# Kernel optimization log

Hardware: AMD Instinct MI355X
Metric: run time of the kernel (lower is better)

The kernel has to match this reference:

```python
import jax, jax.numpy as jnp
import numpy as np

B, T, D, E = 8, 512, 128, 256

def setup_inputs() -> dict:
    key = jax.random.key(0)
    ks = jax.random.split(key, 6)
    s_d = 1.0 / np.sqrt(D)
    return {
        "x": jax.random.normal(ks[0], (B, T, D), jnp.float32),
        "Wg": jax.random.normal(ks[1], (D, E), jnp.float32) * s_d,
        "bg": jnp.zeros((E,), jnp.float32),
        "expert_w": jax.random.normal(ks[2], (E, D, D), jnp.float32) * s_d,
        "w1": jax.random.normal(ks[3], (D, D), jnp.float32) * s_d,
        "b1": jnp.zeros((D,), jnp.float32),
        "w2": jax.random.normal(ks[4], (D, D), jnp.float32) * s_d,
        "b2": jnp.zeros((D,), jnp.float32),
    }

def reference(x, Wg, bg, expert_w, w1, b1, w2, b2):
    n_experts = expert_w.shape[0]
    # router (context=None -> route on x itself)
    gate_scores = jax.nn.softmax(x @ Wg + bg, axis=-1)            # [B,T,E]
    top_vals, top_idx = jax.lax.top_k(gate_scores, 2)             # [B,T,2]
    top_w = top_vals / (jnp.sum(top_vals, axis=-1, keepdims=True) + 1e-6)
    # dense per-expert projection (faithful to original einsum over ALL experts)
    expert_outputs = jnp.einsum('btd,edo->bteo', x, expert_w)     # [B,T,E,D]
    # top-2 one-hot mask with normalized weights -> [B,T,E]
    mask = jnp.sum(jax.nn.one_hot(top_idx, n_experts, dtype=x.dtype) * top_w[..., None], axis=2)
    mixed = jnp.einsum('bteo,bte->bto', expert_outputs, mask)     # [B,T,D]
    # SwiGLU
    g = mixed @ w1 + b1
    weighted_avg = g * jax.nn.sigmoid(g) * (mixed @ w2 + b2)      # [B,T,D]
    # variance consensus against swiglu output
    diff_sq = jnp.square(expert_outputs - weighted_avg[:, :, None, :])
    weighted_var = jnp.einsum('bteo,bte->bto', diff_sq, mask)     # [B,T,D]
    consensus = jnp.exp(-jnp.mean(weighted_var, axis=-1))         # [B,T]
    return weighted_avg, consensus
```

## Files before the change

### kernel.cpp

```cpp
#include <hip/hip_runtime.h>
#include <math.h>

#define NT  4096
#define DD  128
#define EE  256

__global__ __launch_bounds__(256) void router_kernel(
    const float* __restrict__ x, const float* __restrict__ Wg,
    const float* __restrict__ bg, float2* __restrict__ ww,
    int2* __restrict__ sel)
{
    const int bid = blockIdx.x;
    const int tid = threadIdx.x;
    const int t0  = bid * 8;

    __shared__ float xt[DD][8];
    __shared__ float lg[8][EE];

    {
        const int q = tid >> 5, part = tid & 31;
        const float4 v = *(reinterpret_cast<const float4*>(
            x + (size_t)(t0 + q) * DD) + part);
        xt[part * 4 + 0][q] = v.x;
        xt[part * 4 + 1][q] = v.y;
        xt[part * 4 + 2][q] = v.z;
        xt[part * 4 + 3][q] = v.w;
    }
    __syncthreads();

    {
        const int e = tid;
        const float be = bg[e];
        float a0 = be, a1 = be, a2 = be, a3 = be;
        float a4 = be, a5 = be, a6 = be, a7 = be;
        #pragma unroll 8
        for (int d = 0; d < DD; ++d) {
            const float w = Wg[(size_t)d * EE + e];
            const float4 xa = *reinterpret_cast<const float4*>(&xt[d][0]);
            const float4 xb = *reinterpret_cast<const float4*>(&xt[d][4]);
            a0 = fmaf(xa.x, w, a0);  a1 = fmaf(xa.y, w, a1);
            a2 = fmaf(xa.z, w, a2);  a3 = fmaf(xa.w, w, a3);
            a4 = fmaf(xb.x, w, a4);  a5 = fmaf(xb.y, w, a5);
            a6 = fmaf(xb.z, w, a6);  a7 = fmaf(xb.w, w, a7);
        }
        lg[0][e] = a0;  lg[1][e] = a1;  lg[2][e] = a2;  lg[3][e] = a3;
        lg[4][e] = a4;  lg[5][e] = a5;  lg[6][e] = a6;  lg[7][e] = a7;
    }
    __syncthreads();

    const int lane = tid & 63;
    const int wv   = tid >> 6;
    #pragma unroll
    for (int rep = 0; rep < 2; ++rep) {
        const int tk = wv * 2 + rep;
        const int t  = t0 + tk;
        const float4 lv = *reinterpret_cast<const float4*>(&lg[tk][lane * 4]);
        float v[4] = {lv.x, lv.y, lv.z, lv.w};

        float m = v[0]; int mi = lane * 4;
        #pragma unroll
        for (int j = 1; j < 4; ++j)
            if (v[j] > m) { m = v[j]; mi = lane * 4 + j; }
        #pragma unroll
        for (int s = 32; s; s >>= 1) {
            const float om = __shfl_xor(m, s);
            const int   oi = __shfl_xor(mi, s);
            if (om > m || (om == m && oi < mi)) { m = om; mi = oi; }
        }

        float ssum = 0.0f;
        #pragma unroll
        for (int j = 0; j < 4; ++j) ssum += __expf(v[j] - m);
        #pragma unroll
        for (int s = 32; s; s >>= 1) ssum += __shfl_xor(ssum, s);

        float m2 = -INFINITY; int mi2 = 0;
        #pragma unroll
        for (int j = 0; j < 4; ++j) {
            const int ei = lane * 4 + j;
            if (ei != mi && v[j] > m2) { m2 = v[j]; mi2 = ei; }
        }
        #pragma unroll
        for (int s = 32; s; s >>= 1) {
            const float om = __shfl_xor(m2, s);
            const int   oi = __shfl_xor(mi2, s);
            if (om > m2 || (om == m2 && oi < mi2)) { m2 = om; mi2 = oi; }
        }

        if (lane == 0) {
            const float p1 = 1.0f / ssum;
            const float p2 = __expf(m2 - m) / ssum;
            const float den = p1 + p2 + 1e-6f;
            ww[t]  = make_float2(p1 / den, p2 / den);
            sel[t] = make_int2(mi, mi2);
        }
    }
}

__global__ __launch_bounds__(128) void expert_kernel(
    const float* __restrict__ x, const float* __restrict__ ew,
    const int2* __restrict__ sel, float* __restrict__ ybuf)
{
    const int wg = (blockIdx.x & 7) * 128 + (blockIdx.x >> 3);
    const int e  = wg >> 2;
    const int c  = wg & 3;
    const int tid = threadIdx.x;

    __shared__ float xt[DD][8];
    __shared__ int   lst[128];
    __shared__ int   lcnt;
    if (tid == 0) lcnt = 0;
    __syncthreads();

    const int tbase = c * 1024;
    #pragma unroll
    for (int it = 0; it < 8; ++it) {
        const int tok = tbase + it * 128 + tid;
        const int2 s = sel[tok];
        if (s.x == e) { const int p = atomicAdd(&lcnt, 1); if (p < 128) lst[p] = 2 * tok; }
        if (s.y == e) { const int p = atomicAdd(&lcnt, 1); if (p < 128) lst[p] = 2 * tok + 1; }
    }
    __syncthreads();
    int n = lcnt;
    if (n > 128) n = 128;
    if (n == 0) return;

    const int o = tid;
    const float* W = ew + (size_t)e * DD * DD;

    for (int base = 0; base < n; base += 8) {
        {
            const int q = tid >> 4, part = tid & 15;
            if (base + q < n) {
                const int fi = lst[base + q];
                const float4* xr = reinterpret_cast<const float4*>(
                    x + (size_t)(fi >> 1) * DD) + part * 2;
                const float4 u0 = xr[0], u1 = xr[1];
                xt[part * 8 + 0][q] = u0.x;  xt[part * 8 + 1][q] = u0.y;
                xt[part * 8 + 2][q] = u0.z;  xt[part * 8 + 3][q] = u0.w;
                xt[part * 8 + 4][q] = u1.x;  xt[part * 8 + 5][q] = u1.y;
                xt[part * 8 + 6][q] = u1.z;  xt[part * 8 + 7][q] = u1.w;
            }
        }
        __syncthreads();

        float a0 = 0.f, a1 = 0.f, a2 = 0.f, a3 = 0.f;
        float a4 = 0.f, a5 = 0.f, a6 = 0.f, a7 = 0.f;
        #pragma unroll 8
        for (int d = 0; d < DD; ++d) {
            const float w = W[(size_t)d * DD + o];
            const float4 xa = *reinterpret_cast<const float4*>(&xt[d][0]);
            const float4 xb = *reinterpret_cast<const float4*>(&xt[d][4]);
            a0 = fmaf(xa.x, w, a0);  a1 = fmaf(xa.y, w, a1);
            a2 = fmaf(xa.z, w, a2);  a3 = fmaf(xa.w, w, a3);
            a4 = fmaf(xb.x, w, a4);  a5 = fmaf(xb.y, w, a5);
            a6 = fmaf(xb.z, w, a6);  a7 = fmaf(xb.w, w, a7);
        }

        if (base + 0 < n) ybuf[(size_t)lst[base + 0] * DD + o] = a0;
        if (base + 1 < n) ybuf[(size_t)lst[base + 1] * DD + o] = a1;
        if (base + 2 < n) ybuf[(size_t)lst[base + 2] * DD + o] = a2;
        if (base + 3 < n) ybuf[(size_t)lst[base + 3] * DD + o] = a3;
        if (base + 4 < n) ybuf[(size_t)lst[base + 4] * DD + o] = a4;
        if (base + 5 < n) ybuf[(size_t)lst[base + 5] * DD + o] = a5;
        if (base + 6 < n) ybuf[(size_t)lst[base + 6] * DD + o] = a6;
        if (base + 7 < n) ybuf[(size_t)lst[base + 7] * DD + o] = a7;
        __syncthreads();
    }
}

__global__ __launch_bounds__(256) void swiglu_kernel(
    const float* __restrict__ ybuf, const float2* __restrict__ ww,
    const float* __restrict__ w1, const float* __restrict__ b1,
    const float* __restrict__ w2, const float* __restrict__ b2,
    float* __restrict__ out_avg, float* __restrict__ out_cons)
{
    const int tid = threadIdx.x;
    const int t0  = blockIdx.x * 8;

    __shared__ float mt[DD][8];
    __shared__ float gh[2][8][DD];

    {
        const int q = tid >> 5, part = tid & 31;
        const int t = t0 + q;
        const float2 w = ww[t];
        const float4 a = *(reinterpret_cast<const float4*>(
            ybuf + (size_t)(2 * t) * DD) + part);
        const float4 b = *(reinterpret_cast<const float4*>(
            ybuf + (size_t)(2 * t + 1) * DD) + part);
        mt[part * 4 + 0][q] = w.x * a.x + w.y * b.x;
        mt[part * 4 + 1][q] = w.x * a.y + w.y * b.y;
        mt[part * 4 + 2][q] = w.x * a.z + w.y * b.z;
        mt[part * 4 + 3][q] = w.x * a.w + w.y * b.w;
    }
    __syncthreads();

    {
        const int o = tid & 127, h = tid >> 7;
        const float* Wc = h ? w2 : w1;
        const float bias = h ? b2[o] : b1[o];
        float a0 = bias, a1 = bias, a2 = bias, a3 = bias;
        float a4 = bias, a5 = bias, a6 = bias, a7 = bias;
        #pragma unroll 8
        for (int d = 0; d < DD; ++d) {
            const float w = Wc[(size_t)d * DD + o];
            const float4 xa = *reinterpret_cast<const float4*>(&mt[d][0]);
            const float4 xb = *reinterpret_cast<const float4*>(&mt[d][4]);
            a0 = fmaf(xa.x, w, a0);  a1 = fmaf(xa.y, w, a1);
            a2 = fmaf(xa.z, w, a2);  a3 = fmaf(xa.w, w, a3);
            a4 = fmaf(xb.x, w, a4);  a5 = fmaf(xb.y, w, a5);
            a6 = fmaf(xb.z, w, a6);  a7 = fmaf(xb.w, w, a7);
        }
        gh[h][0][o] = a0;  gh[h][1][o] = a1;  gh[h][2][o] = a2;  gh[h][3][o] = a3;
        gh[h][4][o] = a4;  gh[h][5][o] = a5;  gh[h][6][o] = a6;  gh[h][7][o] = a7;
    }
    __syncthreads();

    {
        const int q = tid >> 5, part = tid & 31;
        const int t = t0 + q;
        const float2 w = ww[t];
        const float4 a = *(reinterpret_cast<const float4*>(
            ybuf + (size_t)(2 * t) * DD) + part);
        const float4 b = *(reinterpret_cast<const float4*>(
            ybuf + (size_t)(2 * t + 1) * DD) + part);
        const float4 gv = *reinterpret_cast<const float4*>(&gh[0][q][part * 4]);
        const float4 hv = *reinterpret_cast<const float4*>(&gh[1][q][part * 4]);

        float4 r; float v = 0.0f;
        {
            const float g = gv.x, sig = 1.0f / (1.0f + __expf(-g));
            r.x = g * sig * hv.x;
            const float da = a.x - r.x, db = b.x - r.x;
            v += w.x * da * da + w.y * db * db;
        }
        {
            const float g = gv.y, sig = 1.0f / (1.0f + __expf(-g));
            r.y = g * sig * hv.y;
            const float da = a.y - r.y, db = b.y - r.y;
            v += w.x * da * da + w.y * db * db;
        }
        {
            const float g = gv.z, sig = 1.0f / (1.0f + __expf(-g));
            r.z = g * sig * hv.z;
            const float da = a.z - r.z, db = b.z - r.z;
            v += w.x * da * da + w.y * db * db;
        }
        {
            const float g = gv.w, sig = 1.0f / (1.0f + __expf(-g));
            r.w = g * sig * hv.w;
            const float da = a.w - r.w, db = b.w - r.w;
            v += w.x * da * da + w.y * db * db;
        }
        *(reinterpret_cast<float4*>(out_avg + (size_t)t * DD) + part) = r;

        #pragma unroll
        for (int s = 16; s; s >>= 1) v += __shfl_down(v, s);
        if (part == 0) out_cons[t] = __expf(-v * (1.0f / DD));
    }
}

extern "C" void kernel_launch(void* const* d_in, const int* in_sizes, int n_in,
                              void* d_out, int out_size, void* d_ws, size_t ws_size,
                              hipStream_t stream) {
    const float* x   = (const float*)d_in[0];
    const float* Wg  = (const float*)d_in[1];
    const float* bg  = (const float*)d_in[2];
    const float* ew  = (const float*)d_in[3];
    const float* w1  = (const float*)d_in[4];
    const float* b1  = (const float*)d_in[5];
    const float* w2  = (const float*)d_in[6];
    const float* b2  = (const float*)d_in[7];

    float* out_avg  = (float*)d_out;
    float* out_cons = out_avg + (size_t)NT * DD;

    char* ws = (char*)d_ws;
    float*  ybuf = (float*)ws;
    float2* wwp  = (float2*)(ws + 4 * 1024 * 1024);
    int2*   selp = (int2*)  (ws + 4 * 1024 * 1024 + 32 * 1024);

    router_kernel<<<NT / 8, 256, 0, stream>>>(x, Wg, bg, wwp, selp);
    expert_kernel<<<EE * 4, 128, 0, stream>>>(x, ew, selp, ybuf);
    swiglu_kernel<<<NT / 8, 256, 0, stream>>>(ybuf, wwp, w1, b1, w2, b2,
                                              out_avg, out_cons);
}
```

Before: 49.61 us.

## Process each expert in one 256-thread block instead of four token-chunk blocks

The expert kernel now launches one block per expert that scans all tokens, instead of four blocks per expert each scanning a quarter of the tokens. Each block runs 256 threads that compute two 8-token groups against the same expert weight columns. The aim is to cut redundant reads of each 64KB expert weight matrix and reduce launch overhead. In exchange, the per-expert token list is still capped at 128, now for the whole expert rather than per chunk, so an expert with more than 128 routed tokens would overflow. There is also more serial work per block with fewer blocks overall.

```diff
diff --git a/kernel.cpp b/kernel.cpp
--- a/kernel.cpp
+++ b/kernel.cpp
@@ -97,25 +97,22 @@
     }
 }
 
-__global__ __launch_bounds__(128) void expert_kernel(
+__global__ __launch_bounds__(256) void expert_kernel(
     const float* __restrict__ x, const float* __restrict__ ew,
     const int2* __restrict__ sel, float* __restrict__ ybuf)
 {
-    const int wg = (blockIdx.x & 7) * 128 + (blockIdx.x >> 3);
-    const int e  = wg >> 2;
-    const int c  = wg & 3;
+    const int e   = (blockIdx.x & 7) * 32 + (blockIdx.x >> 3);
     const int tid = threadIdx.x;
 
-    __shared__ float xt[DD][8];
+    __shared__ float xt[DD][16];
     __shared__ int   lst[128];
     __shared__ int   lcnt;
     if (tid == 0) lcnt = 0;
     __syncthreads();
 
-    const int tbase = c * 1024;
     #pragma unroll
-    for (int it = 0; it < 8; ++it) {
-        const int tok = tbase + it * 128 + tid;
+    for (int it = 0; it < 16; ++it) {
+        const int tok = it * 256 + tid;
         const int2 s = sel[tok];
         if (s.x == e) { const int p = atomicAdd(&lcnt, 1); if (p < 128) lst[p] = 2 * tok; }
         if (s.y == e) { const int p = atomicAdd(&lcnt, 1); if (p < 128) lst[p] = 2 * tok + 1; }
@@ -123,12 +120,12 @@
     __syncthreads();
     int n = lcnt;
     if (n > 128) n = 128;
-    if (n == 0) return;
-
-    const int o = tid;
+
+    const int o   = tid & 127;
+    const int str = tid >> 7;
     const float* W = ew + (size_t)e * DD * DD;
 
-    for (int base = 0; base < n; base += 8) {
+    for (int base = 0; base < n; base += 16) {
         {
             const int q = tid >> 4, part = tid & 15;
             if (base + q < n) {
@@ -144,27 +141,29 @@
         }
         __syncthreads();
 
+        const int rq = str * 8;
         float a0 = 0.f, a1 = 0.f, a2 = 0.f, a3 = 0.f;
         float a4 = 0.f, a5 = 0.f, a6 = 0.f, a7 = 0.f;
         #pragma unroll 8
         for (int d = 0; d < DD; ++d) {
             const float w = W[(size_t)d * DD + o];
-            const float4 xa = *reinterpret_cast<const float4*>(&xt[d][0]);
-            const float4 xb = *reinterpret_cast<const float4*>(&xt[d][4]);
+            const float4 xa = *reinterpret_cast<const float4*>(&xt[d][rq]);
+            const float4 xb = *reinterpret_cast<const float4*>(&xt[d][rq + 4]);
             a0 = fmaf(xa.x, w, a0);  a1 = fmaf(xa.y, w, a1);
             a2 = fmaf(xa.z, w, a2);  a3 = fmaf(xa.w, w, a3);
             a4 = fmaf(xb.x, w, a4);  a5 = fmaf(xb.y, w, a5);
             a6 = fmaf(xb.z, w, a6);  a7 = fmaf(xb.w, w, a7);
         }
 
-        if (base + 0 < n) ybuf[(size_t)lst[base + 0] * DD + o] = a0;
-        if (base + 1 < n) ybuf[(size_t)lst[base + 1] * DD + o] = a1;
-        if (base + 2 < n) ybuf[(size_t)lst[base + 2] * DD + o] = a2;
-        if (base + 3 < n) ybuf[(size_t)lst[base + 3] * DD + o] = a3;
-        if (base + 4 < n) ybuf[(size_t)lst[base + 4] * DD + o] = a4;
-        if (base + 5 < n) ybuf[(size_t)lst[base + 5] * DD + o] = a5;
-        if (base + 6 < n) ybuf[(size_t)lst[base + 6] * DD + o] = a6;
-        if (base + 7 < n) ybuf[(size_t)lst[base + 7] * DD + o] = a7;
+        const int rb = base + rq;
+        if (rb + 0 < n) ybuf[(size_t)lst[rb + 0] * DD + o] = a0;
+        if (rb + 1 < n) ybuf[(size_t)lst[rb + 1] * DD + o] = a1;
+        if (rb + 2 < n) ybuf[(size_t)lst[rb + 2] * DD + o] = a2;
+        if (rb + 3 < n) ybuf[(size_t)lst[rb + 3] * DD + o] = a3;
+        if (rb + 4 < n) ybuf[(size_t)lst[rb + 4] * DD + o] = a4;
+        if (rb + 5 < n) ybuf[(size_t)lst[rb + 5] * DD + o] = a5;
+        if (rb + 6 < n) ybuf[(size_t)lst[rb + 6] * DD + o] = a6;
+        if (rb + 7 < n) ybuf[(size_t)lst[rb + 7] * DD + o] = a7;
         __syncthreads();
     }
 }
@@ -282,7 +281,7 @@
     int2*   selp = (int2*)  (ws + 4 * 1024 * 1024 + 32 * 1024);
 
     router_kernel<<<NT / 8, 256, 0, stream>>>(x, Wg, bg, wwp, selp);
-    expert_kernel<<<EE * 4, 128, 0, stream>>>(x, ew, selp, ybuf);
+    expert_kernel<<<EE, 256, 0, stream>>>(x, ew, selp, ybuf);
     swiglu_kernel<<<NT / 8, 256, 0, stream>>>(ybuf, wwp, w1, b1, w2, b2,
                                               out_avg, out_cons);
 }
```

Result: slower. 55.62 us (+12.1%).
